# Optimization experiments

Hardware: AMD Instinct MI355X
Metric: run time of the kernel (lower is better)

The kernel has to match this reference:

```python
import jax, jax.numpy as jnp
import numpy as np

B, N = 4096, 2048


def _nrmse(o, t):
    # o, t: [B, 1, N]. Per-sample RMSE over all non-batch elements,
    # normalized by per-sample (max - min) of the target.
    rmse = jnp.sqrt(jnp.mean((o - t) ** 2, axis=(1, 2)))        # [B]
    rng = jnp.max(t, axis=(1, 2)) - jnp.min(t, axis=(1, 2))     # [B]
    return rmse / rng


def setup_inputs() -> dict:
    key = jax.random.key(0)
    ks = jax.random.split(key, 6)
    names = ["o1", "t1", "o2", "t2", "o3", "t3"]
    return {n: jax.random.normal(k, (B, 1, N), dtype=jnp.float32) for n, k in zip(names, ks)}


def reference(o1, t1, o2, t2, o3, t3):
    loss = (0.5 * _nrmse(o1, t1)
            + 0.25 * _nrmse(o2, t2)
            + 0.25 * _nrmse(o3, t3))  # [B]
    return jnp.mean(loss)
```

## Files before the change

### kernel.cpp

```cpp
#include <hip/hip_runtime.h>
#include <math.h>

constexpr int N_ELEM = 2048;
constexpr int BATCH  = 4096;
constexpr int BLOCK  = 256;
constexpr int TASKS  = 3 * BATCH;
constexpr int GRID1  = TASKS / (BLOCK / 64);

__global__ __launch_bounds__(BLOCK)
void wnrmse_stage1(const float* __restrict__ o1, const float* __restrict__ t1,
                   const float* __restrict__ o2, const float* __restrict__ t2,
                   const float* __restrict__ o3, const float* __restrict__ t3,
                   float* __restrict__ partial)
{
    const int tid  = threadIdx.x;
    const int wave = tid >> 6;
    const int lane = tid & 63;
    const int task = blockIdx.x * (BLOCK / 64) + wave;

    const int pair = task >> 12;
    const int row  = task & (BATCH - 1);

    const float* ob = (pair == 0) ? o1 : ((pair == 1) ? o2 : o3);
    const float* tb = (pair == 0) ? t1 : ((pair == 1) ? t2 : t3);
    const float  wgt = (pair == 0) ? 0.50f : 0.25f;

    const float4* o4 = (const float4*)(ob + (size_t)row * N_ELEM) + lane;
    const float4* t4 = (const float4*)(tb + (size_t)row * N_ELEM) + lane;

    float4 ov[8], tv[8];
#pragma unroll
    for (int j = 0; j < 8; ++j) ov[j] = o4[j * 64];
#pragma unroll
    for (int j = 0; j < 8; ++j) tv[j] = t4[j * 64];

    float ssd0 = 0.0f, ssd1 = 0.0f;
    float tmax0 = -INFINITY, tmax1 = -INFINITY;
    float tmin0 =  INFINITY, tmin1 =  INFINITY;
#pragma unroll
    for (int j = 0; j < 8; ++j) {
        float d0 = ov[j].x - tv[j].x;
        float d1 = ov[j].y - tv[j].y;
        float d2 = ov[j].z - tv[j].z;
        float d3 = ov[j].w - tv[j].w;
        ssd0 += d0 * d0 + d1 * d1;
        ssd1 += d2 * d2 + d3 * d3;
        tmax0 = fmaxf(tmax0, fmaxf(tv[j].x, tv[j].y));
        tmax1 = fmaxf(tmax1, fmaxf(tv[j].z, tv[j].w));
        tmin0 = fminf(tmin0, fminf(tv[j].x, tv[j].y));
        tmin1 = fminf(tmin1, fminf(tv[j].z, tv[j].w));
    }
    float ssd  = ssd0 + ssd1;
    float tmax = fmaxf(tmax0, tmax1);
    float tmin = fminf(tmin0, tmin1);

#pragma unroll
    for (int off = 32; off > 0; off >>= 1) {
        ssd  += __shfl_xor(ssd, off, 64);
        tmax  = fmaxf(tmax, __shfl_xor(tmax, off, 64));
        tmin  = fminf(tmin, __shfl_xor(tmin, off, 64));
    }

    const float rmse  = sqrtf(ssd * (1.0f / (float)N_ELEM));
    const float local = wgt * rmse / (tmax - tmin);

    __shared__ float s_part[BLOCK / 64];
    if (lane == 0) s_part[wave] = local;
    __syncthreads();
    if (tid == 0) {
        partial[blockIdx.x] = s_part[0] + s_part[1] + s_part[2] + s_part[3];
    }
}

__global__ __launch_bounds__(BLOCK)
void wnrmse_stage2(const float* __restrict__ partial, float* __restrict__ out)
{
    const int tid = threadIdx.x;
    float s = 0.0f;
    for (int i = tid; i < GRID1; i += BLOCK) s += partial[i];

#pragma unroll
    for (int off = 32; off > 0; off >>= 1) s += __shfl_xor(s, off, 64);

    __shared__ float s_part[BLOCK / 64];
    const int wave = tid >> 6;
    const int lane = tid & 63;
    if (lane == 0) s_part[wave] = s;
    __syncthreads();
    if (tid == 0) {
        float tot = s_part[0] + s_part[1] + s_part[2] + s_part[3];
        out[0] = tot * (1.0f / (float)BATCH);
    }
}

extern "C" void kernel_launch(void* const* d_in, const int* in_sizes, int n_in,
                              void* d_out, int out_size, void* d_ws, size_t ws_size,
                              hipStream_t stream) {
    const float* o1 = (const float*)d_in[0];
    const float* t1 = (const float*)d_in[1];
    const float* o2 = (const float*)d_in[2];
    const float* t2 = (const float*)d_in[3];
    const float* o3 = (const float*)d_in[4];
    const float* t3 = (const float*)d_in[5];
    float* out     = (float*)d_out;
    float* partial = (float*)d_ws;

    wnrmse_stage1<<<GRID1, BLOCK, 0, stream>>>(o1, t1, o2, t2, o3, t3, partial);
    wnrmse_stage2<<<1, BLOCK, 0, stream>>>(partial, out);
}
```

Before: 206.7 us.

## Split rows into column segments with per-lane rows and cross-segment reduction

```diff
diff --git a/kernel.cpp b/kernel.cpp
--- a/kernel.cpp
+++ b/kernel.cpp
@@ -1,95 +1,96 @@
 #include <hip/hip_runtime.h>
 #include <math.h>
 
-constexpr int N_ELEM = 2048;
-constexpr int BATCH  = 4096;
-constexpr int BLOCK  = 256;
-constexpr int TASKS  = 3 * BATCH;
-constexpr int GRID1  = TASKS / (BLOCK / 64);
+constexpr int N_ELEM   = 2048;
+constexpr int BATCH    = 4096;
+constexpr int ROWS     = 3 * BATCH;
+constexpr int SEG      = 16;
+constexpr int SEG_COLS = N_ELEM / SEG;
+constexpr int BLOCK    = 256;
+constexpr int WTASKS   = (ROWS / 64) * SEG;
+constexpr int GRID1    = WTASKS / (BLOCK / 64);
 
 __global__ __launch_bounds__(BLOCK)
 void wnrmse_stage1(const float* __restrict__ o1, const float* __restrict__ t1,
                    const float* __restrict__ o2, const float* __restrict__ t2,
                    const float* __restrict__ o3, const float* __restrict__ t3,
-                   float* __restrict__ partial)
+                   float* __restrict__ pssd, float* __restrict__ pmax,
+                   float* __restrict__ pmin)
 {
     const int tid  = threadIdx.x;
     const int wave = tid >> 6;
     const int lane = tid & 63;
-    const int task = blockIdx.x * (BLOCK / 64) + wave;
-
-    const int pair = task >> 12;
-    const int row  = task & (BATCH - 1);
+    const int w    = blockIdx.x * (BLOCK / 64) + wave;
+    const int g    = w >> 4;
+    const int s    = w & (SEG - 1);
+    const int r    = g * 64 + lane;
+    const int pair = g >> 6;
+    const int row  = r & (BATCH - 1);
 
     const float* ob = (pair == 0) ? o1 : ((pair == 1) ? o2 : o3);
     const float* tb = (pair == 0) ? t1 : ((pair == 1) ? t2 : t3);
-    const float  wgt = (pair == 0) ? 0.50f : 0.25f;
 
-    const float4* o4 = (const float4*)(ob + (size_t)row * N_ELEM) + lane;
-    const float4* t4 = (const float4*)(tb + (size_t)row * N_ELEM) + lane;
-
-    float4 ov[8], tv[8];
-#pragma unroll
-    for (int j = 0; j < 8; ++j) ov[j] = o4[j * 64];
-#pragma unroll
-    for (int j = 0; j < 8; ++j) tv[j] = t4[j * 64];
+    const float4* o4 = (const float4*)(ob + (size_t)row * N_ELEM + s * SEG_COLS);
+    const float4* t4 = (const float4*)(tb + (size_t)row * N_ELEM + s * SEG_COLS);
 
     float ssd0 = 0.0f, ssd1 = 0.0f;
-    float tmax0 = -INFINITY, tmax1 = -INFINITY;
-    float tmin0 =  INFINITY, tmin1 =  INFINITY;
-#pragma unroll
-    for (int j = 0; j < 8; ++j) {
-        float d0 = ov[j].x - tv[j].x;
-        float d1 = ov[j].y - tv[j].y;
-        float d2 = ov[j].z - tv[j].z;
-        float d3 = ov[j].w - tv[j].w;
-        ssd0 += d0 * d0 + d1 * d1;
-        ssd1 += d2 * d2 + d3 * d3;
-        tmax0 = fmaxf(tmax0, fmaxf(tv[j].x, tv[j].y));
-        tmax1 = fmaxf(tmax1, fmaxf(tv[j].z, tv[j].w));
-        tmin0 = fminf(tmin0, fminf(tv[j].x, tv[j].y));
-        tmin1 = fminf(tmin1, fminf(tv[j].z, tv[j].w));
-    }
-    float ssd  = ssd0 + ssd1;
-    float tmax = fmaxf(tmax0, tmax1);
-    float tmin = fminf(tmin0, tmin1);
+    float mx0 = -INFINITY, mx1 = -INFINITY;
+    float mn0 =  INFINITY, mn1 =  INFINITY;
 
 #pragma unroll
-    for (int off = 32; off > 0; off >>= 1) {
-        ssd  += __shfl_xor(ssd, off, 64);
-        tmax  = fmaxf(tmax, __shfl_xor(tmax, off, 64));
-        tmin  = fminf(tmin, __shfl_xor(tmin, off, 64));
+    for (int jg = 0; jg < SEG_COLS / 16; ++jg) {
+        float4 a0 = o4[4 * jg + 0], a1 = o4[4 * jg + 1];
+        float4 a2 = o4[4 * jg + 2], a3 = o4[4 * jg + 3];
+        float4 b0 = t4[4 * jg + 0], b1 = t4[4 * jg + 1];
+        float4 b2 = t4[4 * jg + 2], b3 = t4[4 * jg + 3];
+#define ACC1(AV, BV)                                              \
+        {                                                         \
+            float d0 = AV.x - BV.x, d1 = AV.y - BV.y;             \
+            float d2 = AV.z - BV.z, d3 = AV.w - BV.w;             \
+            ssd0 += d0 * d0 + d1 * d1;                            \
+            ssd1 += d2 * d2 + d3 * d3;                            \
+            mx0 = fmaxf(mx0, fmaxf(BV.x, BV.y));                  \
+            mx1 = fmaxf(mx1, fmaxf(BV.z, BV.w));                  \
+            mn0 = fminf(mn0, fminf(BV.x, BV.y));                  \
+            mn1 = fminf(mn1, fminf(BV.z, BV.w));                  \
+        }
+        ACC1(a0, b0) ACC1(a1, b1) ACC1(a2, b2) ACC1(a3, b3)
+#undef ACC1
     }
 
-    const float rmse  = sqrtf(ssd * (1.0f / (float)N_ELEM));
-    const float local = wgt * rmse / (tmax - tmin);
-
-    __shared__ float s_part[BLOCK / 64];
-    if (lane == 0) s_part[wave] = local;
-    __syncthreads();
-    if (tid == 0) {
-        partial[blockIdx.x] = s_part[0] + s_part[1] + s_part[2] + s_part[3];
-    }
+    pssd[s * ROWS + r] = ssd0 + ssd1;
+    pmax[s * ROWS + r] = fmaxf(mx0, mx1);
+    pmin[s * ROWS + r] = fminf(mn0, mn1);
 }
 
-__global__ __launch_bounds__(BLOCK)
-void wnrmse_stage2(const float* __restrict__ partial, float* __restrict__ out)
+__global__ __launch_bounds__(1024)
+void wnrmse_stage2(const float* __restrict__ pssd, const float* __restrict__ pmax,
+                   const float* __restrict__ pmin, float* __restrict__ out)
 {
     const int tid = threadIdx.x;
-    float s = 0.0f;
-    for (int i = tid; i < GRID1; i += BLOCK) s += partial[i];
+    float acc = 0.0f;
+    for (int r = tid; r < ROWS; r += 1024) {
+        float ssd = 0.0f, mx = -INFINITY, mn = INFINITY;
+#pragma unroll
+        for (int s2 = 0; s2 < SEG; ++s2) {
+            ssd += pssd[s2 * ROWS + r];
+            mx   = fmaxf(mx, pmax[s2 * ROWS + r]);
+            mn   = fminf(mn, pmin[s2 * ROWS + r]);
+        }
+        const float wgt = ((r >> 12) == 0) ? 0.50f : 0.25f;
+        acc += wgt * sqrtf(ssd * (1.0f / (float)N_ELEM)) / (mx - mn);
+    }
 
 #pragma unroll
-    for (int off = 32; off > 0; off >>= 1) s += __shfl_xor(s, off, 64);
-
-    __shared__ float s_part[BLOCK / 64];
-    const int wave = tid >> 6;
-    const int lane = tid & 63;
-    if (lane == 0) s_part[wave] = s;
+    for (int off = 32; off > 0; off >>= 1) acc += __shfl_xor(acc, off, 64);
+    __shared__ float sp[16];
+    if ((tid & 63) == 0) sp[tid >> 6] = acc;
     __syncthreads();
-    if (tid == 0) {
-        float tot = s_part[0] + s_part[1] + s_part[2] + s_part[3];
-        out[0] = tot * (1.0f / (float)BATCH);
+    if (tid < 16) {
+        float v = sp[tid];
+#pragma unroll
+        for (int off = 8; off > 0; off >>= 1) v += __shfl_xor(v, off, 16);
+        if (tid == 0) out[0] = v * (1.0f / (float)BATCH);
     }
 }
 
@@ -102,9 +103,12 @@
     const float* t2 = (const float*)d_in[3];
     const float* o3 = (const float*)d_in[4];
     const float* t3 = (const float*)d_in[5];
-    float* out     = (float*)d_out;
-    float* partial = (float*)d_ws;
+    float* out  = (float*)d_out;
+    float* pssd = (float*)d_ws;
+    float* pmax = pssd + SEG * ROWS;
+    float* pmin = pmax + SEG * ROWS;
 
-    wnrmse_stage1<<<GRID1, BLOCK, 0, stream>>>(o1, t1, o2, t2, o3, t3, partial);
-    wnrmse_stage2<<<1, BLOCK, 0, stream>>>(partial, out);
+    wnrmse_stage1<<<GRID1, BLOCK, 0, stream>>>(o1, t1, o2, t2, o3, t3,
+                                               pssd, pmax, pmin);
+    wnrmse_stage2<<<1, 1024, 0, stream>>>(pssd, pmax, pmin, out);
 }
```

Result: slower. 230.1 us (+11.3%).
